# Performance work log

Hardware: AMD Instinct MI355X
Metric: run time of the kernel (lower is better)

## Reference

```python
import jax, jax.numpy as jnp
import numpy as np

N = 100000   # nodes
E = 1600000  # edges (avg degree 16)
IN = 7       # in_channels
H = 2        # heads
C = 64       # hidden_dim (per-head channels)
NC = 4       # num_classes
SLOPE = 0.2  # PyG GATConv default negative_slope


def gat_layer(x, W, a_src, a_dst, b, src, dst, concat):
    """PyG-style GATConv. x:[n,F], W:[F,H*C], a_*:[H,C], src/dst:[E'] (incl self-loops)."""
    n = x.shape[0]
    h = (x @ W).reshape(n, H, C)                 # [n,H,C]
    es = jnp.sum(h * a_src, axis=-1)             # [n,H] per-node source score
    ed = jnp.sum(h * a_dst, axis=-1)             # [n,H] per-node dest score
    e = jax.nn.leaky_relu(es[src] + ed[dst], SLOPE)          # [E',H]
    m = jax.ops.segment_max(e, dst, num_segments=n)          # stable segment softmax
    p = jnp.exp(e - m[dst])
    s = jax.ops.segment_sum(p, dst, num_segments=n)
    alpha = p / s[dst]                                        # [E',H]
    out = jax.ops.segment_sum(h[src] * alpha[:, :, None], dst, num_segments=n)  # [n,H,C]
    out = out.reshape(n, H * C) if concat else out.mean(axis=1)
    return out + b


def setup_inputs() -> dict:
    key = jax.random.key(0)
    ks = jax.random.split(key, 14)
    sc = 0.2
    return {
        "x": jax.random.normal(ks[0], (N, IN), jnp.float32),
        "edge_index": jax.random.randint(ks[1], (2, E), 0, N, dtype=jnp.int32),
        "W1": jax.random.normal(ks[2], (IN, H * C), jnp.float32) * sc,
        "a_src1": jax.random.normal(ks[3], (H, C), jnp.float32) * sc,
        "a_dst1": jax.random.normal(ks[4], (H, C), jnp.float32) * sc,
        "b1": jnp.zeros((H * C,), jnp.float32),
        "W2": jax.random.normal(ks[5], (H * C, H * C), jnp.float32) * sc,
        "a_src2": jax.random.normal(ks[6], (H, C), jnp.float32) * sc,
        "a_dst2": jax.random.normal(ks[7], (H, C), jnp.float32) * sc,
        "b2": jnp.zeros((C,), jnp.float32),
        "Wc1": jax.random.normal(ks[8], (C, C), jnp.float32) * sc,
        "bc1": jnp.zeros((C,), jnp.float32),
        "Wc2": jax.random.normal(ks[9], (C, NC), jnp.float32) * sc,
        "bc2": jnp.zeros((NC,), jnp.float32),
    }


def reference(x, edge_index, W1, a_src1, a_dst1, b1, W2, a_src2, a_dst2, b2, Wc1, bc1, Wc2, bc2):
    loops = jnp.arange(N, dtype=edge_index.dtype)            # PyG default add_self_loops=True
    src = jnp.concatenate([edge_index[0], loops])
    dst = jnp.concatenate([edge_index[1], loops])
    h = jax.nn.relu(gat_layer(x, W1, a_src1, a_dst1, b1, src, dst, True))   # [N, 128]
    h = gat_layer(h, W2, a_src2, a_dst2, b2, src, dst, False)               # [N, 64]
    return jax.nn.relu(h @ Wc1 + bc1) @ Wc2 + bc2                           # [N, 4]
```

## Files before the change

### kernel.cpp

```cpp
#include <hip/hip_runtime.h>
#include <hip/hip_bf16.h>


#define LRELU_SLOPE 0.2f

__device__ __forceinline__ float wave_red_max(float v) {
#pragma unroll
    for (int o = 32; o > 0; o >>= 1) v = fmaxf(v, __shfl_xor(v, o));
    return v;
}
__device__ __forceinline__ float wave_red_sum(float v) {
#pragma unroll
    for (int o = 32; o > 0; o >>= 1) v += __shfl_xor(v, o);
    return v;
}
__device__ __forceinline__ float lrelu(float v) { return v > 0.f ? v : LRELU_SLOPE * v; }
__device__ __forceinline__ unsigned short f2bf(float f) {
    unsigned int x = __float_as_uint(f);
    return (unsigned short)((x + 0x7fffu + ((x >> 16) & 1u)) >> 16);
}
__device__ __forceinline__ void fma8(float* f, uint4 hv, float a) {
    unsigned u[4] = {hv.x, hv.y, hv.z, hv.w};
#pragma unroll
    for (int i = 0; i < 4; i++) {
        float lo = __uint_as_float(u[i] << 16);
        float hi = __uint_as_float(u[i] & 0xffff0000u);
        f[2 * i]     += lo * a;
        f[2 * i + 1] += hi * a;
    }
}

__global__ void k_hist(const int* __restrict__ dstA, int* __restrict__ cnt, int E) {
    int i = blockIdx.x * 256 + threadIdx.x;
    if (i < E) atomicAdd(&cnt[dstA[i]], 1);
}

__global__ void k_scan1(const int* __restrict__ cnt, int* __restrict__ rs,
                        int* __restrict__ part, int n) {
    __shared__ int sm[256];
    int t = threadIdx.x;
    int i = blockIdx.x * 256 + t;
    int v = (i < n) ? cnt[i] : 0;
    sm[t] = v;
    __syncthreads();
#pragma unroll
    for (int off = 1; off < 256; off <<= 1) {
        int x = (t >= off) ? sm[t - off] : 0;
        __syncthreads();
        sm[t] += x;
        __syncthreads();
    }
    if (i < n) rs[i] = sm[t] - v;
    if (t == 255) part[blockIdx.x] = sm[255];
}

__global__ void k_scan2(int* part, int np) {
    __shared__ int sm[512];
    int t = threadIdx.x;
    int v = (t < np) ? part[t] : 0;
    sm[t] = v;
    __syncthreads();
#pragma unroll
    for (int off = 1; off < 512; off <<= 1) {
        int x = (t >= off) ? sm[t - off] : 0;
        __syncthreads();
        sm[t] += x;
        __syncthreads();
    }
    if (t < np) part[t] = sm[t] - v;
}

__global__ void k_scan3(int* rs, const int* __restrict__ part, int n, int total) {
    int i = blockIdx.x * 256 + threadIdx.x;
    if (i < n) rs[i] += part[blockIdx.x];
    if (i == 0) rs[n] = total;
}

__global__ void k_scatter(const int* __restrict__ srcA, const int* __restrict__ dstA,
                          const int* __restrict__ rs, int* __restrict__ cur,
                          int* __restrict__ ssrc, int E) {
    int i = blockIdx.x * 256 + threadIdx.x;
    if (i < E) {
        int d = dstA[i];
        int p = atomicAdd(&cur[d], 1);
        ssrc[rs[d] + p] = srcA[i];
    }
}

__global__ void k_prep(const float* __restrict__ W1, const float* __restrict__ as1,
                       const float* __restrict__ ad1, const float* __restrict__ W2,
                       const float* __restrict__ as2, const float* __restrict__ ad2,
                       float* __restrict__ ws1, float* __restrict__ wd1,
                       float* __restrict__ ws2, float* __restrict__ wd2) {
    int t = threadIdx.x;
    int k = t >> 1, h = t & 1;
    float s = 0.f, d = 0.f;
    for (int cc = 0; cc < 64; cc++) {
        float w = W2[k * 128 + h * 64 + cc];
        s += w * as2[h * 64 + cc];
        d += w * ad2[h * 64 + cc];
    }
    ws2[t] = s;
    wd2[t] = d;
    if (t < 14) {
        int kk = t >> 1, hh = t & 1;
        float s1 = 0.f, d1 = 0.f;
        for (int cc = 0; cc < 64; cc++) {
            float w = W1[kk * 128 + hh * 64 + cc];
            s1 += w * as1[hh * 64 + cc];
            d1 += w * ad1[hh * 64 + cc];
        }
        ws1[t] = s1;
        wd1[t] = d1;
    }
}

__global__ void k_feat1(const float* __restrict__ x, const float* __restrict__ W1,
                        const float* __restrict__ ws1, const float* __restrict__ wd1,
                        unsigned short* __restrict__ h1, float* __restrict__ es1,
                        float* __restrict__ ed1, int n) {
    int node = blockIdx.x;
    int c = threadIdx.x;
    float xv[7];
#pragma unroll
    for (int k = 0; k < 7; k++) xv[k] = x[node * 7 + k];
    float acc = 0.f;
#pragma unroll
    for (int k = 0; k < 7; k++) acc += xv[k] * W1[k * 128 + c];
    h1[(size_t)node * 128 + c] = f2bf(acc);
    if (c < 2) {
        float s = 0.f;
#pragma unroll
        for (int k = 0; k < 7; k++) s += xv[k] * ws1[k * 2 + c];
        es1[node * 2 + c] = s;
    } else if (c < 4) {
        int h = c - 2;
        float s = 0.f;
#pragma unroll
        for (int k = 0; k < 7; k++) s += xv[k] * wd1[k * 2 + h];
        ed1[node * 2 + h] = s;
    }
}

template <int LAYER>
__global__ void k_aggr(const unsigned short* __restrict__ h, const float* __restrict__ es,
                       const float* __restrict__ ed, const int* __restrict__ rs,
                       const int* __restrict__ ssrc, const float* __restrict__ bias,
                       float* __restrict__ out, const float* __restrict__ ws2,
                       const float* __restrict__ wd2, float* __restrict__ es2,
                       float* __restrict__ ed2, const float* __restrict__ Wc1,
                       const float* __restrict__ bc1, const float* __restrict__ Wc2,
                       const float* __restrict__ bc2, int n) {
    int wid = threadIdx.x >> 6, lane = threadIdx.x & 63;
    int node = blockIdx.x * 4 + wid;
    if (node >= n) return;
    int grp = lane >> 4, sub = lane & 15;
    int base = sub * 8;
    int hd = sub >> 3;
    int beg = rs[node], deg = rs[node + 1] - beg;
    float2 edv = *(const float2*)&ed[node * 2];
    float2 esn = *(const float2*)&es[node * 2];
    float e0s = lrelu(esn.x + edv.x);
    float e1s = lrelu(esn.y + edv.y);
    float f[8] = {0.f, 0.f, 0.f, 0.f, 0.f, 0.f, 0.f, 0.f};

    if (deg <= 64) {
        bool valid = lane < deg;
        int sv = valid ? ssrc[beg + lane] : 0;
        float2 ev; ev.x = 0.f; ev.y = 0.f;
        if (valid) ev = *(const float2*)&es[sv * 2];
        float e0 = valid ? lrelu(ev.x + edv.x) : -3.0e38f;
        float e1 = valid ? lrelu(ev.y + edv.y) : -3.0e38f;
        float m0 = fmaxf(wave_red_max(e0), e0s);
        float m1 = fmaxf(wave_red_max(e1), e1s);
        float p0 = valid ? __expf(e0 - m0) : 0.f;
        float p1 = valid ? __expf(e1 - m1) : 0.f;
        float exs0 = __expf(e0s - m0), exs1 = __expf(e1s - m1);
        float inv0 = 1.f / (wave_red_sum(p0) + exs0);
        float inv1 = 1.f / (wave_red_sum(p1) + exs1);
        float a0 = p0 * inv0, a1 = p1 * inv1;
        if (grp == 0) {
            float aself = hd ? exs1 * inv1 : exs0 * inv0;
            uint4 hvs = *(const uint4*)&h[(size_t)node * 128 + base];
            fma8(f, hvs, aself);
        }
        int j = 0;
        for (; j + 8 <= deg; j += 8) {
            int jj0 = j + grp, jj1 = j + 4 + grp;
            int s0v = __shfl(sv, jj0), s1v = __shfl(sv, jj1);
            float b00 = __shfl(a0, jj0), b10 = __shfl(a1, jj0);
            float b01 = __shfl(a0, jj1), b11 = __shfl(a1, jj1);
            float av0 = hd ? b10 : b00;
            float av1 = hd ? b11 : b01;
            uint4 h0 = *(const uint4*)&h[(size_t)s0v * 128 + base];
            uint4 h1 = *(const uint4*)&h[(size_t)s1v * 128 + base];
            fma8(f, h0, av0);
            fma8(f, h1, av1);
        }
        for (; j < deg; j += 4) {
            int jj = j + grp;
            int sjv = __shfl(sv, jj);
            float b0 = __shfl(a0, jj), b1 = __shfl(a1, jj);
            float av = hd ? b1 : b0;
            uint4 hv = *(const uint4*)&h[(size_t)sjv * 128 + base];
            fma8(f, hv, av);
        }
    } else {
        float m0 = e0s, s0 = 1.f, m1 = e1s, s1 = 1.f;
        for (int c0 = 0; c0 < deg; c0 += 64) {
            int i = c0 + lane;
            bool val = i < deg;
            int sv = val ? ssrc[beg + i] : 0;
            float e0 = val ? lrelu(es[sv * 2 + 0] + edv.x) : -3.0e38f;
            float e1 = val ? lrelu(es[sv * 2 + 1] + edv.y) : -3.0e38f;
            float nm0 = fmaxf(m0, wave_red_max(e0));
            float nm1 = fmaxf(m1, wave_red_max(e1));
            float p0 = val ? __expf(e0 - nm0) : 0.f;
            float p1 = val ? __expf(e1 - nm1) : 0.f;
            s0 = s0 * __expf(m0 - nm0) + wave_red_sum(p0);
            s1 = s1 * __expf(m1 - nm1) + wave_red_sum(p1);
            m0 = nm0; m1 = nm1;
        }
        float inv0 = 1.f / s0, inv1 = 1.f / s1;
        if (grp == 0) {
            float aself = hd ? __expf(e1s - m1) * inv1 : __expf(e0s - m0) * inv0;
            uint4 hvs = *(const uint4*)&h[(size_t)node * 128 + base];
            fma8(f, hvs, aself);
        }
        for (int c0 = 0; c0 < deg; c0 += 64) {
            int i = c0 + lane;
            bool val = i < deg;
            int svc = val ? ssrc[beg + i] : 0;
            float a0c = 0.f, a1c = 0.f;
            if (val) {
                float e0 = lrelu(es[svc * 2 + 0] + edv.x);
                float e1 = lrelu(es[svc * 2 + 1] + edv.y);
                a0c = __expf(e0 - m0) * inv0;
                a1c = __expf(e1 - m1) * inv1;
            }
            int cnt = min(64, deg - c0);
            for (int jl = 0; jl < cnt; jl += 4) {
                int jj = jl + grp;
                int sjv = __shfl(svc, jj);
                float b0 = __shfl(a0c, jj), b1 = __shfl(a1c, jj);
                float av = hd ? b1 : b0;
                uint4 hv = *(const uint4*)&h[(size_t)sjv * 128 + base];
                fma8(f, hv, av);
            }
        }
    }

#pragma unroll
    for (int r = 0; r < 8; r++) {
        f[r] += __shfl_xor(f[r], 16);
        f[r] += __shfl_xor(f[r], 32);
    }

    if (LAYER == 1) {
        float o[8];
#pragma unroll
        for (int r = 0; r < 8; r++) o[r] = fmaxf(f[r] + bias[base + r], 0.f);
        if (grp == 0) {
            float4 v0 = {o[0], o[1], o[2], o[3]};
            float4 v1 = {o[4], o[5], o[6], o[7]};
            *(float4*)&out[(size_t)node * 128 + base] = v0;
            *(float4*)&out[(size_t)node * 128 + base + 4] = v1;
        }
        float s0 = 0.f, s1 = 0.f, d0 = 0.f, d1 = 0.f;
#pragma unroll
        for (int r = 0; r < 8; r++) {
            float2 wsv = *(const float2*)&ws2[(base + r) * 2];
            float2 wdv = *(const float2*)&wd2[(base + r) * 2];
            s0 += o[r] * wsv.x; s1 += o[r] * wsv.y;
            d0 += o[r] * wdv.x; d1 += o[r] * wdv.y;
        }
        s0 = wave_red_sum(s0) * 0.25f;
        s1 = wave_red_sum(s1) * 0.25f;
        d0 = wave_red_sum(d0) * 0.25f;
        d1 = wave_red_sum(d1) * 0.25f;
        if (lane == 0) {
            float2 sv2; sv2.x = s0; sv2.y = s1;
            float2 dv2; dv2.x = d0; dv2.y = d1;
            *(float2*)&es2[node * 2] = sv2;
            *(float2*)&ed2[node * 2] = dv2;
        }
    } else {
        float p[8];
#pragma unroll
        for (int r = 0; r < 8; r++) p[r] = __shfl_xor(f[r], 8);
        float o2[8];
#pragma unroll
        for (int r = 0; r < 8; r++)
            o2[r] = 0.5f * (f[r] + p[r]) + bias[(base & 63) + r];
        float yc = bc1[lane];
#pragma unroll
        for (int k = 0; k < 64; k++) {
            float ov = __shfl(o2[k & 7], k >> 3);
            yc += ov * Wc1[k * 64 + lane];
        }
        float y = fmaxf(yc, 0.f);
        float4 w2v = *(const float4*)&Wc2[lane * 4];
        float p0 = y * w2v.x, p1 = y * w2v.y, p2 = y * w2v.z, p3 = y * w2v.w;
        p0 = wave_red_sum(p0); p1 = wave_red_sum(p1);
        p2 = wave_red_sum(p2); p3 = wave_red_sum(p3);
        if (lane == 0) {
            float4 o; o.x = p0 + bc2[0]; o.y = p1 + bc2[1];
            o.z = p2 + bc2[2]; o.w = p3 + bc2[3];
            *(float4*)&out[(size_t)node * 4] = o;
        }
    }
}

__global__ void k_gemm2(const float* __restrict__ A, const float* __restrict__ B,
                        unsigned short* __restrict__ C, int M) {
    __shared__ float As[32][65];
    __shared__ float Bs[32][132];
    int bm = blockIdx.x * 64;
    int t = threadIdx.x;
    int tx = t & 31;
    int ty = t >> 5;
    float acc[8][4];
#pragma unroll
    for (int i = 0; i < 8; i++)
#pragma unroll
        for (int j = 0; j < 4; j++) acc[i][j] = 0.f;

    for (int k0 = 0; k0 < 128; k0 += 32) {
        int lk = t & 31, lm = t >> 5;
#pragma unroll
        for (int p = 0; p < 8; p++) {
            int m = lm + p * 8;
            int row = bm + m;
            As[lk][m] = (row < M) ? A[(size_t)row * 128 + k0 + lk] : 0.f;
        }
        int bn = t & 127, bk = t >> 7;
#pragma unroll
        for (int p = 0; p < 16; p++) {
            Bs[bk + p * 2][bn] = B[(k0 + bk + p * 2) * 128 + bn];
        }
        __syncthreads();
#pragma unroll
        for (int k = 0; k < 32; k++) {
            float a[8];
#pragma unroll
            for (int i = 0; i < 8; i++) a[i] = As[k][ty * 8 + i];
            float4 bv = *(const float4*)&Bs[k][tx * 4];
            float b[4] = {bv.x, bv.y, bv.z, bv.w};
#pragma unroll
            for (int i = 0; i < 8; i++)
#pragma unroll
                for (int j = 0; j < 4; j++) acc[i][j] += a[i] * b[j];
        }
        __syncthreads();
    }
#pragma unroll
    for (int i = 0; i < 8; i++) {
        int row = bm + ty * 8 + i;
        if (row < M) {
            ushort4 v;
            v.x = f2bf(acc[i][0]); v.y = f2bf(acc[i][1]);
            v.z = f2bf(acc[i][2]); v.w = f2bf(acc[i][3]);
            *(ushort4*)&C[(size_t)row * 128 + tx * 4] = v;
        }
    }
}

extern "C" void kernel_launch(void* const* d_in, const int* in_sizes, int n_in,
                              void* d_out, int out_size, void* d_ws, size_t ws_size,
                              hipStream_t stream) {
    const float* x   = (const float*)d_in[0];
    const int*   ei  = (const int*)d_in[1];
    const float* W1  = (const float*)d_in[2];
    const float* as1 = (const float*)d_in[3];
    const float* ad1 = (const float*)d_in[4];
    const float* b1  = (const float*)d_in[5];
    const float* W2  = (const float*)d_in[6];
    const float* as2 = (const float*)d_in[7];
    const float* ad2 = (const float*)d_in[8];
    const float* b2  = (const float*)d_in[9];
    const float* Wc1 = (const float*)d_in[10];
    const float* bc1 = (const float*)d_in[11];
    const float* Wc2 = (const float*)d_in[12];
    const float* bc2 = (const float*)d_in[13];
    float* out = (float*)d_out;

    int n = in_sizes[0] / 7;
    int E = in_sizes[1] / 2;
    const int* srcA = ei;
    const int* dstA = ei + E;

    char* ws = (char*)d_ws;
    size_t off = 0;
    auto alloc = [&](size_t bytes) -> char* {
        char* p = ws + off;
        off += (bytes + 255) & ~(size_t)255;
        return p;
    };
    unsigned short* bufH = (unsigned short*)alloc((size_t)n * 128 * 2);
    float* bufO = (float*)alloc((size_t)n * 128 * 4);
    float* es1  = (float*)alloc((size_t)n * 2 * 4);
    float* ed1  = (float*)alloc((size_t)n * 2 * 4);
    float* es2  = (float*)alloc((size_t)n * 2 * 4);
    float* ed2  = (float*)alloc((size_t)n * 2 * 4);
    float* ws1  = (float*)alloc(64);
    float* wd1  = (float*)alloc(64);
    float* ws2v = (float*)alloc(256 * 4);
    float* wd2v = (float*)alloc(256 * 4);
    int* rs   = (int*)alloc((size_t)(n + 1) * 4);
    int* cnt  = (int*)alloc((size_t)n * 4);
    int* part = (int*)alloc(512 * 4);
    int* ssrc = (int*)alloc((size_t)E * 4);

    int eb = (E + 255) / 256;
    int nb = (n + 255) / 256;

    hipMemsetAsync(cnt, 0, (size_t)n * 4, stream);
    k_hist<<<eb, 256, 0, stream>>>(dstA, cnt, E);
    k_scan1<<<nb, 256, 0, stream>>>(cnt, rs, part, n);
    k_scan2<<<1, 512, 0, stream>>>(part, nb);
    k_scan3<<<nb, 256, 0, stream>>>(rs, part, n, E);
    hipMemsetAsync(cnt, 0, (size_t)n * 4, stream);
    k_scatter<<<eb, 256, 0, stream>>>(srcA, dstA, rs, cnt, ssrc, E);

    k_prep<<<1, 256, 0, stream>>>(W1, as1, ad1, W2, as2, ad2, ws1, wd1, ws2v, wd2v);
    k_feat1<<<n, 128, 0, stream>>>(x, W1, ws1, wd1, bufH, es1, ed1, n);
    k_aggr<1><<<(n + 3) / 4, 256, 0, stream>>>(bufH, es1, ed1, rs, ssrc, b1, bufO,
                                               ws2v, wd2v, es2, ed2,
                                               nullptr, nullptr, nullptr, nullptr, n);
    k_gemm2<<<(n + 63) / 64, 256, 0, stream>>>(bufO, W2, bufH, n);
    k_aggr<2><<<(n + 3) / 4, 256, 0, stream>>>(bufH, es2, ed2, rs, ssrc, b2, out,
                                               nullptr, nullptr, nullptr, nullptr,
                                               Wc1, bc1, Wc2, bc2, n);
}
```

Before: 603.5 us.

## Split attention softmax into separate kernel writing per-edge alpha records

Adds a k_alpha kernel that computes the per-edge softmax coefficients and stores them with the source index as 16-byte records, plus a per-node self-loop coefficient. The aggregation kernel then reads these records directly instead of running reductions and shuffles before gathering features. This is meant to shorten the aggregation kernel's dependency chain and remove the shuffle overhead. In exchange it adds an extra launch per layer and extra global memory traffic for writing and reading the record buffer.

```diff
diff --git a/kernel.cpp b/kernel.cpp
--- a/kernel.cpp
+++ b/kernel.cpp
@@ -142,27 +142,17 @@
     }
 }
 
-template <int LAYER>
-__global__ void k_aggr(const unsigned short* __restrict__ h, const float* __restrict__ es,
-                       const float* __restrict__ ed, const int* __restrict__ rs,
-                       const int* __restrict__ ssrc, const float* __restrict__ bias,
-                       float* __restrict__ out, const float* __restrict__ ws2,
-                       const float* __restrict__ wd2, float* __restrict__ es2,
-                       float* __restrict__ ed2, const float* __restrict__ Wc1,
-                       const float* __restrict__ bc1, const float* __restrict__ Wc2,
-                       const float* __restrict__ bc2, int n) {
+__global__ void k_alpha(const float* __restrict__ es, const float* __restrict__ ed,
+                        const int* __restrict__ rs, const int* __restrict__ ssrc,
+                        uint4* __restrict__ rec, float2* __restrict__ aself, int n) {
     int wid = threadIdx.x >> 6, lane = threadIdx.x & 63;
     int node = blockIdx.x * 4 + wid;
     if (node >= n) return;
-    int grp = lane >> 4, sub = lane & 15;
-    int base = sub * 8;
-    int hd = sub >> 3;
     int beg = rs[node], deg = rs[node + 1] - beg;
     float2 edv = *(const float2*)&ed[node * 2];
     float2 esn = *(const float2*)&es[node * 2];
     float e0s = lrelu(esn.x + edv.x);
     float e1s = lrelu(esn.y + edv.y);
-    float f[8] = {0.f, 0.f, 0.f, 0.f, 0.f, 0.f, 0.f, 0.f};
 
     if (deg <= 64) {
         bool valid = lane < deg;
@@ -178,32 +168,13 @@
         float exs0 = __expf(e0s - m0), exs1 = __expf(e1s - m1);
         float inv0 = 1.f / (wave_red_sum(p0) + exs0);
         float inv1 = 1.f / (wave_red_sum(p1) + exs1);
-        float a0 = p0 * inv0, a1 = p1 * inv1;
-        if (grp == 0) {
-            float aself = hd ? exs1 * inv1 : exs0 * inv0;
-            uint4 hvs = *(const uint4*)&h[(size_t)node * 128 + base];
-            fma8(f, hvs, aself);
-        }
-        int j = 0;
-        for (; j + 8 <= deg; j += 8) {
-            int jj0 = j + grp, jj1 = j + 4 + grp;
-            int s0v = __shfl(sv, jj0), s1v = __shfl(sv, jj1);
-            float b00 = __shfl(a0, jj0), b10 = __shfl(a1, jj0);
-            float b01 = __shfl(a0, jj1), b11 = __shfl(a1, jj1);
-            float av0 = hd ? b10 : b00;
-            float av1 = hd ? b11 : b01;
-            uint4 h0 = *(const uint4*)&h[(size_t)s0v * 128 + base];
-            uint4 h1 = *(const uint4*)&h[(size_t)s1v * 128 + base];
-            fma8(f, h0, av0);
-            fma8(f, h1, av1);
-        }
-        for (; j < deg; j += 4) {
-            int jj = j + grp;
-            int sjv = __shfl(sv, jj);
-            float b0 = __shfl(a0, jj), b1 = __shfl(a1, jj);
-            float av = hd ? b1 : b0;
-            uint4 hv = *(const uint4*)&h[(size_t)sjv * 128 + base];
-            fma8(f, hv, av);
+        if (valid)
+            rec[beg + lane] = make_uint4((unsigned)sv,
+                                         __float_as_uint(p0 * inv0),
+                                         __float_as_uint(p1 * inv1), 0u);
+        if (lane == 0) {
+            float2 a; a.x = exs0 * inv0; a.y = exs1 * inv1;
+            aself[node] = a;
         }
     } else {
         float m0 = e0s, s0 = 1.f, m1 = e1s, s1 = 1.f;
@@ -222,32 +193,61 @@
             m0 = nm0; m1 = nm1;
         }
         float inv0 = 1.f / s0, inv1 = 1.f / s1;
-        if (grp == 0) {
-            float aself = hd ? __expf(e1s - m1) * inv1 : __expf(e0s - m0) * inv0;
-            uint4 hvs = *(const uint4*)&h[(size_t)node * 128 + base];
-            fma8(f, hvs, aself);
-        }
         for (int c0 = 0; c0 < deg; c0 += 64) {
             int i = c0 + lane;
-            bool val = i < deg;
-            int svc = val ? ssrc[beg + i] : 0;
-            float a0c = 0.f, a1c = 0.f;
-            if (val) {
-                float e0 = lrelu(es[svc * 2 + 0] + edv.x);
-                float e1 = lrelu(es[svc * 2 + 1] + edv.y);
-                a0c = __expf(e0 - m0) * inv0;
-                a1c = __expf(e1 - m1) * inv1;
+            if (i < deg) {
+                int sv = ssrc[beg + i];
+                float e0 = lrelu(es[sv * 2 + 0] + edv.x);
+                float e1 = lrelu(es[sv * 2 + 1] + edv.y);
+                rec[beg + i] = make_uint4((unsigned)sv,
+                                          __float_as_uint(__expf(e0 - m0) * inv0),
+                                          __float_as_uint(__expf(e1 - m1) * inv1), 0u);
             }
-            int cnt = min(64, deg - c0);
-            for (int jl = 0; jl < cnt; jl += 4) {
-                int jj = jl + grp;
-                int sjv = __shfl(svc, jj);
-                float b0 = __shfl(a0c, jj), b1 = __shfl(a1c, jj);
-                float av = hd ? b1 : b0;
-                uint4 hv = *(const uint4*)&h[(size_t)sjv * 128 + base];
-                fma8(f, hv, av);
-            }
-        }
+        }
+        if (lane == 0) {
+            float2 a; a.x = __expf(e0s - m0) * inv0; a.y = __expf(e1s - m1) * inv1;
+            aself[node] = a;
+        }
+    }
+}
+
+template <int LAYER>
+__global__ void k_aggr(const unsigned short* __restrict__ h, const int* __restrict__ rs,
+                       const uint4* __restrict__ rec, const float2* __restrict__ aself,
+                       const float* __restrict__ bias, float* __restrict__ out,
+                       const float* __restrict__ ws2, const float* __restrict__ wd2,
+                       float* __restrict__ es2, float* __restrict__ ed2,
+                       const float* __restrict__ Wc1, const float* __restrict__ bc1,
+                       const float* __restrict__ Wc2, const float* __restrict__ bc2,
+                       int n) {
+    int wid = threadIdx.x >> 6, lane = threadIdx.x & 63;
+    int node = blockIdx.x * 4 + wid;
+    if (node >= n) return;
+    int grp = lane >> 4, sub = lane & 15;
+    int base = sub * 8;
+    int hd = sub >> 3;
+    int beg = rs[node], deg = rs[node + 1] - beg;
+    float f[8] = {0.f, 0.f, 0.f, 0.f, 0.f, 0.f, 0.f, 0.f};
+
+    if (grp == 0) {
+        float2 as = aself[node];
+        float a = hd ? as.y : as.x;
+        uint4 hvs = *(const uint4*)&h[(size_t)node * 128 + base];
+        fma8(f, hvs, a);
+    }
+    int j = grp;
+    for (; j + 4 < deg; j += 8) {
+        uint4 r0 = rec[beg + j];
+        uint4 r1 = rec[beg + j + 4];
+        uint4 h0 = *(const uint4*)&h[(size_t)(int)r0.x * 128 + base];
+        uint4 h1v = *(const uint4*)&h[(size_t)(int)r1.x * 128 + base];
+        fma8(f, h0, hd ? __uint_as_float(r0.z) : __uint_as_float(r0.y));
+        fma8(f, h1v, hd ? __uint_as_float(r1.z) : __uint_as_float(r1.y));
+    }
+    if (j < deg) {
+        uint4 r = rec[beg + j];
+        uint4 hv = *(const uint4*)&h[(size_t)(int)r.x * 128 + base];
+        fma8(f, hv, hd ? __uint_as_float(r.z) : __uint_as_float(r.y));
     }
 
 #pragma unroll
@@ -410,6 +410,8 @@
     int* cnt  = (int*)alloc((size_t)n * 4);
     int* part = (int*)alloc(512 * 4);
     int* ssrc = (int*)alloc((size_t)E * 4);
+    uint4* rec = (uint4*)alloc((size_t)E * 16);
+    float2* aself = (float2*)alloc((size_t)n * 8);
 
     int eb = (E + 255) / 256;
     int nb = (n + 255) / 256;
@@ -424,11 +426,13 @@
 
     k_prep<<<1, 256, 0, stream>>>(W1, as1, ad1, W2, as2, ad2, ws1, wd1, ws2v, wd2v);
     k_feat1<<<n, 128, 0, stream>>>(x, W1, ws1, wd1, bufH, es1, ed1, n);
-    k_aggr<1><<<(n + 3) / 4, 256, 0, stream>>>(bufH, es1, ed1, rs, ssrc, b1, bufO,
+    k_alpha<<<(n + 3) / 4, 256, 0, stream>>>(es1, ed1, rs, ssrc, rec, aself, n);
+    k_aggr<1><<<(n + 3) / 4, 256, 0, stream>>>(bufH, rs, rec, aself, b1, bufO,
                                                ws2v, wd2v, es2, ed2,
                                                nullptr, nullptr, nullptr, nullptr, n);
     k_gemm2<<<(n + 63) / 64, 256, 0, stream>>>(bufO, W2, bufH, n);
-    k_aggr<2><<<(n + 3) / 4, 256, 0, stream>>>(bufH, es2, ed2, rs, ssrc, b2, out,
+    k_alpha<<<(n + 3) / 4, 256, 0, stream>>>(es2, ed2, rs, ssrc, rec, aself, n);
+    k_aggr<2><<<(n + 3) / 4, 256, 0, stream>>>(bufH, rs, rec, aself, b2, out,
                                                nullptr, nullptr, nullptr, nullptr,
                                                Wc1, bc1, Wc2, bc2, n);
 }
```

New measurement: 625.6 us. 3.7% more time.
